# Performance work log

Hardware: AMD Instinct MI355X
Metric: run time of the kernel (lower is better)

The kernel has to match this reference:

```python
import jax, jax.numpy as jnp
import numpy as np

B, N, D = 128, 512, 256
NUM_TYPES, NUM_STATS = 6, 8
W_TYPE, W_STATS, W_CORR = 1.0, 1.0, 0.5
LN_EPS = 1e-5


def _mlp_head(x, W1, b1, g, be, W2, b2):
    # Linear -> GELU(exact) -> LayerNorm -> Linear (dropout is identity in eval)
    h = x @ W1 + b1
    h = jax.nn.gelu(h, approximate=False)
    mu = jnp.mean(h, axis=-1, keepdims=True)
    var = jnp.var(h, axis=-1, keepdims=True)
    h = (h - mu) / jnp.sqrt(var + LN_EPS) * g + be
    return h @ W2 + b2


def _masked_mean(x, m):
    m = m.astype(x.dtype)
    return jnp.sum(x * m) / jnp.maximum(jnp.sum(m), 1.0)


def setup_inputs() -> dict:
    key = jax.random.key(0)
    ks = jax.random.split(key, 16)
    s = 1.0 / np.sqrt(D)
    return {
        'column_embeddings': jax.random.normal(ks[0], (B, N, D), jnp.float32),
        'masked_columns': jax.random.uniform(ks[1], (B, N)) < 0.15,
        'type_targets': jax.random.randint(ks[2], (B, N), 0, NUM_TYPES),
        'column_statistics': jax.random.normal(ks[3], (B, N, NUM_STATS), jnp.float32),
        'column_correlations': jax.random.normal(ks[4], (B, N, N), jnp.float32),
        # type head params
        'Wt1': jax.random.normal(ks[5], (D, D), jnp.float32) * s,
        'bt1': jnp.zeros((D,), jnp.float32),
        'gt': jnp.ones((D,), jnp.float32),
        'blt': jnp.zeros((D,), jnp.float32),
        'Wt2': jax.random.normal(ks[6], (D, NUM_TYPES), jnp.float32) * s,
        'bt2': jnp.zeros((NUM_TYPES,), jnp.float32),
        # stats head params
        'Ws1': jax.random.normal(ks[7], (D, D), jnp.float32) * s,
        'bs1': jnp.zeros((D,), jnp.float32),
        'gs': jnp.ones((D,), jnp.float32),
        'bls': jnp.zeros((D,), jnp.float32),
        'Ws2': jax.random.normal(ks[8], (D, NUM_STATS), jnp.float32) * s,
        'bs2': jnp.zeros((NUM_STATS,), jnp.float32),
        # bilinear correlation head (nn.Bilinear(d,d,1) weight [1,d,d] -> [d,d])
        'Wc': jax.random.normal(ks[9], (D, D), jnp.float32) * s,
        'bc': jnp.zeros((), jnp.float32),
    }


def reference(column_embeddings, masked_columns, type_targets, column_statistics,
              column_correlations, Wt1, bt1, gt, blt, Wt2, bt2,
              Ws1, bs1, gs, bls, Ws2, bs2, Wc, bc):
    x = column_embeddings
    m = masked_columns

    type_logits = _mlp_head(x, Wt1, bt1, gt, blt, Wt2, bt2)   # [B,N,6]
    stats_preds = _mlp_head(x, Ws1, bs1, gs, bls, Ws2, bs2)   # [B,N,8]

    # fused bilinear correlation: replaces the O(N^2) python loop
    scores = jnp.einsum('bid,de,bje->bij', x, Wc, x) + bc     # [B,N,N]
    corr = jnp.tanh(scores)
    eye = jnp.eye(N, dtype=bool)
    corr = jnp.where(eye, jnp.ones((), corr.dtype), corr)

    # type loss: masked-mean cross-entropy
    logp = jax.nn.log_softmax(type_logits, axis=-1)
    nll = -jnp.take_along_axis(logp, type_targets[..., None], axis=-1)[..., 0]
    type_loss = _masked_mean(nll, m)

    # stats loss: masked-mean MSE over all stat elements of masked columns
    se = (stats_preds - column_statistics) ** 2
    stats_loss = _masked_mean(se, jnp.broadcast_to(m[:, :, None], se.shape))

    # correlation loss: mask is union over row/col masked columns
    m2 = m[:, :, None] | m[:, None, :]
    corr_loss = _masked_mean((corr - column_correlations) ** 2, m2)

    total = W_TYPE * type_loss + W_STATS * stats_loss + W_CORR * corr_loss
    return total
```

## Files before the change

### kernel.cpp

```cpp
#include <hip/hip_runtime.h>
#include <hip/hip_bf16.h>

#define BB 128
#define NN 512
#define DD 256

typedef __attribute__((ext_vector_type(4))) float f32x4;
typedef __attribute__((ext_vector_type(8))) short s16x8;
typedef __attribute__((ext_vector_type(8))) __bf16 bf16x8;

static __device__ __forceinline__ bf16x8 as_bf(s16x8 v) {
  return __builtin_bit_cast(bf16x8, v);
}

static __device__ __forceinline__ unsigned short f2bf(float f) {
  unsigned u = __builtin_bit_cast(unsigned, f);
  u += 0x7FFFu + ((u >> 16) & 1u);
  return (unsigned short)(u >> 16);
}

__device__ __forceinline__ float wave_sum(float v) {
#pragma unroll
  for (int o = 32; o > 0; o >>= 1) v += __shfl_xor(v, o);
  return v;
}

__global__ void k_init(int* wsi) {
  if (threadIdx.x < 8) wsi[threadIdx.x] = 0;
}

__global__ void k_counts(const int* __restrict__ msk, int* __restrict__ wsi) {
  const int b = blockIdx.x;
  int cnt = 0;
  for (int i = threadIdx.x; i < NN; i += blockDim.x) cnt += (msk[b * NN + i] != 0) ? 1 : 0;
  float s = wave_sum((float)cnt);
  __shared__ float red[4];
  const int lane = threadIdx.x & 63, wv = threadIdx.x >> 6;
  if (lane == 0) red[wv] = s;
  __syncthreads();
  if (threadIdx.x == 0) {
    int k = (int)(red[0] + red[1] + red[2] + red[3] + 0.5f);
    atomicAdd(&wsi[4], k);
    atomicAdd(&wsi[5], NN * NN - (NN - k) * (NN - k));
  }
}

__global__ void k_prep(const float* __restrict__ Wc, const float* __restrict__ Wt1,
                       const float* __restrict__ Ws1, const float* __restrict__ Wt2,
                       const float* __restrict__ Ws2,
                       unsigned short* __restrict__ WcT, unsigned short* __restrict__ Wt1T,
                       unsigned short* __restrict__ Ws1T, unsigned short* __restrict__ Wt2T,
                       unsigned short* __restrict__ Ws2T) {
  int t = blockIdx.x * 256 + threadIdx.x;
  int c = t >> 8, d = t & 255;
  WcT [c * 256 + d] = f2bf(Wc [d * 256 + c]);
  Wt1T[c * 256 + d] = f2bf(Wt1[d * 256 + c]);
  Ws1T[c * 256 + d] = f2bf(Ws1[d * 256 + c]);
  if (c < 16) {
    Wt2T[c * 256 + d] = (c < 6) ? f2bf(Wt2[d * 6 + c]) : (unsigned short)0;
    Ws2T[c * 256 + d] = (c < 8) ? f2bf(Ws2[d * 8 + c]) : (unsigned short)0;
  }
}

__global__ __launch_bounds__(512) void k_heads(
    const float* __restrict__ x, const int* __restrict__ msk,
    const int* __restrict__ tgt, const float* __restrict__ stats,
    const unsigned short* __restrict__ Wt1T, const unsigned short* __restrict__ Ws1T,
    const unsigned short* __restrict__ Wt2T, const unsigned short* __restrict__ Ws2T,
    const float* __restrict__ bt1, const float* __restrict__ bs1,
    const float* __restrict__ gt, const float* __restrict__ gs,
    const float* __restrict__ blt, const float* __restrict__ bls,
    const float* __restrict__ bt2, const float* __restrict__ bs2,
    float* __restrict__ fs)
{
  const int tid = threadIdx.x;
  const int lane = tid & 63, w = tid >> 6;
  const int wm = w & 1, wn = w >> 1;
  const int fr = lane & 15, fg = lane >> 4;
  const int row0 = blockIdx.x * 128;

  __shared__ __align__(16) unsigned short lds_h[128 * 264];
  __shared__ __align__(16) unsigned short lds_a[128 * 72];
  __shared__ __align__(16) unsigned short lds_b[256 * 72];
  __shared__ float sb1[2][256], sg[2][256], sbe[2][256];
  __shared__ float red[128 * 8];
  __shared__ float lg[128 * 16];

  if (tid < 256) { sb1[0][tid] = bt1[tid]; sg[0][tid] = gt[tid]; sbe[0][tid] = blt[tid]; }
  else { int t = tid - 256; sb1[1][t] = bs1[t]; sg[1][t] = gs[t]; sbe[1][t] = bls[t]; }

  f32x4 at[4][4], asx[4][4];
#pragma unroll
  for (int i = 0; i < 4; ++i)
#pragma unroll
    for (int j = 0; j < 4; ++j) {
      at[i][j]  = f32x4{0.f, 0.f, 0.f, 0.f};
      asx[i][j] = f32x4{0.f, 0.f, 0.f, 0.f};
    }

  for (int kt = 0; kt < 4; ++kt) {
    __syncthreads();
#pragma unroll
    for (int p = 0; p < 4; ++p) {
      int idx = tid + p * 512;
      int r = idx >> 4, c4 = idx & 15;
      float4 v = *(const float4*)&x[(size_t)(row0 + r) * DD + kt * 64 + c4 * 4];
      uint2 pk;
      pk.x = (unsigned)f2bf(v.x) | ((unsigned)f2bf(v.y) << 16);
      pk.y = (unsigned)f2bf(v.z) | ((unsigned)f2bf(v.w) << 16);
      *(uint2*)&lds_a[r * 72 + c4 * 4] = pk;
    }
#pragma unroll
    for (int p = 0; p < 4; ++p) {
      int idx = tid + p * 512;
      int r = idx >> 3, ch = idx & 7;
      *(uint4*)&lds_b[r * 72 + ch * 8] = *(const uint4*)&Wt1T[r * 256 + kt * 64 + ch * 8];
    }
    __syncthreads();
#pragma unroll
    for (int ks = 0; ks < 2; ++ks) {
      s16x8 af[4], bfv[4];
#pragma unroll
      for (int i = 0; i < 4; ++i)
        af[i] = *(const s16x8*)&lds_a[(wm * 64 + i * 16 + fr) * 72 + ks * 32 + fg * 8];
#pragma unroll
      for (int j = 0; j < 4; ++j)
        bfv[j] = *(const s16x8*)&lds_b[(wn * 64 + j * 16 + fr) * 72 + ks * 32 + fg * 8];
#pragma unroll
      for (int i = 0; i < 4; ++i)
#pragma unroll
        for (int j = 0; j < 4; ++j)
          at[i][j] = __builtin_amdgcn_mfma_f32_16x16x32_bf16(as_bf(af[i]), as_bf(bfv[j]), at[i][j], 0, 0, 0);
    }
    __syncthreads();
#pragma unroll
    for (int p = 0; p < 4; ++p) {
      int idx = tid + p * 512;
      int r = idx >> 3, ch = idx & 7;
      *(uint4*)&lds_b[r * 72 + ch * 8] = *(const uint4*)&Ws1T[r * 256 + kt * 64 + ch * 8];
    }
    __syncthreads();
#pragma unroll
    for (int ks = 0; ks < 2; ++ks) {
      s16x8 af[4], bfv[4];
#pragma unroll
      for (int i = 0; i < 4; ++i)
        af[i] = *(const s16x8*)&lds_a[(wm * 64 + i * 16 + fr) * 72 + ks * 32 + fg * 8];
#pragma unroll
      for (int j = 0; j < 4; ++j)
        bfv[j] = *(const s16x8*)&lds_b[(wn * 64 + j * 16 + fr) * 72 + ks * 32 + fg * 8];
#pragma unroll
      for (int i = 0; i < 4; ++i)
#pragma unroll
        for (int j = 0; j < 4; ++j)
          asx[i][j] = __builtin_amdgcn_mfma_f32_16x16x32_bf16(as_bf(af[i]), as_bf(bfv[j]), asx[i][j], 0, 0, 0);
    }
  }

  {
    float sA[16], qA[16];
#pragma unroll
    for (int k = 0; k < 16; ++k) { sA[k] = 0.f; qA[k] = 0.f; }
#pragma unroll
    for (int i = 0; i < 4; ++i)
#pragma unroll
      for (int j = 0; j < 4; ++j) {
        int col = wn * 64 + j * 16 + fr;
        float bb = sb1[0][col];
#pragma unroll
        for (int r = 0; r < 4; ++r) {
          float h = at[i][j][r] + bb;
          h = 0.5f * h * (1.0f + erff(h * 0.70710678118654752f));
          at[i][j][r] = h;
          sA[i * 4 + r] += h;
          qA[i * 4 + r] += h * h;
        }
      }
#pragma unroll
    for (int o = 1; o < 16; o <<= 1) {
#pragma unroll
      for (int k = 0; k < 16; ++k) {
        sA[k] += __shfl_xor(sA[k], o);
        qA[k] += __shfl_xor(qA[k], o);
      }
    }
    __syncthreads();
    if (fr == 0) {
#pragma unroll
      for (int i = 0; i < 4; ++i)
#pragma unroll
        for (int r = 0; r < 4; ++r) {
          int row = wm * 64 + i * 16 + fg * 4 + r;
          red[row * 8 + wn]     = sA[i * 4 + r];
          red[row * 8 + 4 + wn] = qA[i * 4 + r];
        }
    }
    __syncthreads();
#pragma unroll
    for (int i = 0; i < 4; ++i)
#pragma unroll
      for (int r = 0; r < 4; ++r) {
        int row = wm * 64 + i * 16 + fg * 4 + r;
        float s = red[row * 8 + 0] + red[row * 8 + 1] + red[row * 8 + 2] + red[row * 8 + 3];
        float q = red[row * 8 + 4] + red[row * 8 + 5] + red[row * 8 + 6] + red[row * 8 + 7];
        float mu = s * (1.0f / DD);
        float var = q * (1.0f / DD) - mu * mu;
        float rstd = rsqrtf(var + 1e-5f);
#pragma unroll
        for (int j = 0; j < 4; ++j) {
          int col = wn * 64 + j * 16 + fr;
          float hn = (at[i][j][r] - mu) * rstd * sg[0][col] + sbe[0][col];
          lds_h[row * 264 + col] = f2bf(hn);
        }
      }
    __syncthreads();
#pragma unroll
    for (int p = 0; p < 2; ++p) {
      int idx = tid + p * 512;
      int r = idx >> 6, c4 = idx & 63;
      *(uint2*)&lds_b[r * 264 + c4 * 4] = *(const uint2*)&Wt2T[r * 256 + c4 * 4];
    }
    __syncthreads();
    {
      f32x4 a1 = f32x4{0.f, 0.f, 0.f, 0.f};
#pragma unroll
      for (int ks = 0; ks < 8; ++ks) {
        s16x8 av = *(const s16x8*)&lds_h[(w * 16 + fr) * 264 + ks * 32 + fg * 8];
        s16x8 bv = *(const s16x8*)&lds_b[fr * 264 + ks * 32 + fg * 8];
        a1 = __builtin_amdgcn_mfma_f32_16x16x32_bf16(as_bf(av), as_bf(bv), a1, 0, 0, 0);
      }
#pragma unroll
      for (int r = 0; r < 4; ++r) lg[(w * 16 + fg * 4 + r) * 16 + fr] = a1[r];
    }
    __syncthreads();
    if (tid < 128) {
      int grow = row0 + tid;
      int mbit = msk[grow];
      float contrib = 0.0f;
      float l[6], mx = -1e30f;
#pragma unroll
      for (int c = 0; c < 6; ++c) { l[c] = lg[tid * 16 + c] + bt2[c]; mx = fmaxf(mx, l[c]); }
      float se = 0.0f;
#pragma unroll
      for (int c = 0; c < 6; ++c) se += expf(l[c] - mx);
      float lse = mx + logf(se);
      int t = tgt[grow];
      float lt = 0.0f;
#pragma unroll
      for (int c = 0; c < 6; ++c) lt = (c == t) ? l[c] : lt;
      contrib = mbit ? (lse - lt) : 0.0f;
      float s = wave_sum(contrib);
      if ((tid & 63) == 0) atomicAdd(&fs[0], s);
    }
    __syncthreads();
  }

  {
    float sA[16], qA[16];
#pragma unroll
    for (int k = 0; k < 16; ++k) { sA[k] = 0.f; qA[k] = 0.f; }
#pragma unroll
    for (int i = 0; i < 4; ++i)
#pragma unroll
      for (int j = 0; j < 4; ++j) {
        int col = wn * 64 + j * 16 + fr;
        float bb = sb1[1][col];
#pragma unroll
        for (int r = 0; r < 4; ++r) {
          float h = asx[i][j][r] + bb;
          h = 0.5f * h * (1.0f + erff(h * 0.70710678118654752f));
          asx[i][j][r] = h;
          sA[i * 4 + r] += h;
          qA[i * 4 + r] += h * h;
        }
      }
#pragma unroll
    for (int o = 1; o < 16; o <<= 1) {
#pragma unroll
      for (int k = 0; k < 16; ++k) {
        sA[k] += __shfl_xor(sA[k], o);
        qA[k] += __shfl_xor(qA[k], o);
      }
    }
    __syncthreads();
    if (fr == 0) {
#pragma unroll
      for (int i = 0; i < 4; ++i)
#pragma unroll
        for (int r = 0; r < 4; ++r) {
          int row = wm * 64 + i * 16 + fg * 4 + r;
          red[row * 8 + wn]     = sA[i * 4 + r];
          red[row * 8 + 4 + wn] = qA[i * 4 + r];
        }
    }
    __syncthreads();
#pragma unroll
    for (int i = 0; i < 4; ++i)
#pragma unroll
      for (int r = 0; r < 4; ++r) {
        int row = wm * 64 + i * 16 + fg * 4 + r;
        float s = red[row * 8 + 0] + red[row * 8 + 1] + red[row * 8 + 2] + red[row * 8 + 3];
        float q = red[row * 8 + 4] + red[row * 8 + 5] + red[row * 8 + 6] + red[row * 8 + 7];
        float mu = s * (1.0f / DD);
        float var = q * (1.0f / DD) - mu * mu;
        float rstd = rsqrtf(var + 1e-5f);
#pragma unroll
        for (int j = 0; j < 4; ++j) {
          int col = wn * 64 + j * 16 + fr;
          float hn = (asx[i][j][r] - mu) * rstd * sg[1][col] + sbe[1][col];
          lds_h[row * 264 + col] = f2bf(hn);
        }
      }
    __syncthreads();
#pragma unroll
    for (int p = 0; p < 2; ++p) {
      int idx = tid + p * 512;
      int r = idx >> 6, c4 = idx & 63;
      *(uint2*)&lds_b[r * 264 + c4 * 4] = *(const uint2*)&Ws2T[r * 256 + c4 * 4];
    }
    __syncthreads();
    {
      f32x4 a1 = f32x4{0.f, 0.f, 0.f, 0.f};
#pragma unroll
      for (int ks = 0; ks < 8; ++ks) {
        s16x8 av = *(const s16x8*)&lds_h[(w * 16 + fr) * 264 + ks * 32 + fg * 8];
        s16x8 bv = *(const s16x8*)&lds_b[fr * 264 + ks * 32 + fg * 8];
        a1 = __builtin_amdgcn_mfma_f32_16x16x32_bf16(as_bf(av), as_bf(bv), a1, 0, 0, 0);
      }
#pragma unroll
      for (int r = 0; r < 4; ++r) lg[(w * 16 + fg * 4 + r) * 16 + fr] = a1[r];
    }
    __syncthreads();
    if (tid < 128) {
      int grow = row0 + tid;
      int mbit = msk[grow];
      const float* st = stats + (size_t)grow * 8;
      float sse = 0.0f;
#pragma unroll
      for (int c = 0; c < 8; ++c) {
        float d = (lg[tid * 16 + c] + bs2[c]) - st[c];
        sse += d * d;
      }
      float contrib = mbit ? sse : 0.0f;
      float s = wave_sum(contrib);
      if ((tid & 63) == 0) atomicAdd(&fs[1], s);
    }
  }
}

__global__ __launch_bounds__(512) void k_corr(
    const float* __restrict__ x, const int* __restrict__ msk,
    const float* __restrict__ corr, const unsigned short* __restrict__ WcT,
    const float* __restrict__ bcp, float* __restrict__ fs)
{
  const int tid = threadIdx.x;
  const int b  = blockIdx.x >> 2;
  const int it = blockIdx.x & 3;
  const int i0 = it * 128;
  const int lane = tid & 63, w = tid >> 6;
  const int wm = w & 1, wn = w >> 1;
  const int fr = lane & 15, fg = lane >> 4;

  __shared__ __align__(16) unsigned short lds_y[128 * 264];
  __shared__ __align__(16) unsigned short lds_a[128 * 72];
  __shared__ __align__(16) unsigned short lds_b[256 * 72];
  __shared__ int ms_i[128];
  __shared__ int ms_j[256];
  __shared__ float red[8];

  const float* xb = x + (size_t)b * NN * DD;

  f32x4 acc[4][4];
#pragma unroll
  for (int i = 0; i < 4; ++i)
#pragma unroll
    for (int j = 0; j < 4; ++j) acc[i][j] = f32x4{0.f, 0.f, 0.f, 0.f};

  for (int kt = 0; kt < 4; ++kt) {
    __syncthreads();
#pragma unroll
    for (int p = 0; p < 4; ++p) {
      int idx = tid + p * 512;
      int r = idx >> 4, c4 = idx & 15;
      float4 v = *(const float4*)&xb[(size_t)(i0 + r) * DD + kt * 64 + c4 * 4];
      uint2 pk;
      pk.x = (unsigned)f2bf(v.x) | ((unsigned)f2bf(v.y) << 16);
      pk.y = (unsigned)f2bf(v.z) | ((unsigned)f2bf(v.w) << 16);
      *(uint2*)&lds_a[r * 72 + c4 * 4] = pk;
    }
#pragma unroll
    for (int p = 0; p < 4; ++p) {
      int idx = tid + p * 512;
      int r = idx >> 3, ch = idx & 7;
      *(uint4*)&lds_b[r * 72 + ch * 8] = *(const uint4*)&WcT[r * 256 + kt * 64 + ch * 8];
    }
    __syncthreads();
#pragma unroll
    for (int ks = 0; ks < 2; ++ks) {
      s16x8 af[4], bfv[4];
#pragma unroll
      for (int i = 0; i < 4; ++i)
        af[i] = *(const s16x8*)&lds_a[(wm * 64 + i * 16 + fr) * 72 + ks * 32 + fg * 8];
#pragma unroll
      for (int j = 0; j < 4; ++j)
        bfv[j] = *(const s16x8*)&lds_b[(wn * 64 + j * 16 + fr) * 72 + ks * 32 + fg * 8];
#pragma unroll
      for (int i = 0; i < 4; ++i)
#pragma unroll
        for (int j = 0; j < 4; ++j)
          acc[i][j] = __builtin_amdgcn_mfma_f32_16x16x32_bf16(as_bf(af[i]), as_bf(bfv[j]), acc[i][j], 0, 0, 0);
    }
  }
#pragma unroll
  for (int i = 0; i < 4; ++i)
#pragma unroll
    for (int j = 0; j < 4; ++j)
#pragma unroll
      for (int r = 0; r < 4; ++r) {
        int row = wm * 64 + i * 16 + fg * 4 + r;
        int col = wn * 64 + j * 16 + fr;
        lds_y[row * 264 + col] = f2bf(acc[i][j][r]);
      }
  if (tid < 128) ms_i[tid] = msk[b * NN + i0 + tid];

  const float bc = bcp[0];
  float sse = 0.0f;

  for (int jc = 0; jc < 2; ++jc) {
    const int j0 = jc * 256;
#pragma unroll
    for (int i = 0; i < 4; ++i)
#pragma unroll
      for (int j = 0; j < 4; ++j) acc[i][j] = f32x4{0.f, 0.f, 0.f, 0.f};

    for (int kt = 0; kt < 4; ++kt) {
      __syncthreads();
#pragma unroll
      for (int p = 0; p < 8; ++p) {
        int idx = tid + p * 512;
        int r = idx >> 4, c4 = idx & 15;
        float4 v = *(const float4*)&xb[(size_t)(j0 + r) * DD + kt * 64 + c4 * 4];
        uint2 pk;
        pk.x = (unsigned)f2bf(v.x) | ((unsigned)f2bf(v.y) << 16);
        pk.y = (unsigned)f2bf(v.z) | ((unsigned)f2bf(v.w) << 16);
        *(uint2*)&lds_b[r * 72 + c4 * 4] = pk;
      }
      if (kt == 0 && tid < 256) ms_j[tid] = msk[b * NN + j0 + tid];
      __syncthreads();
#pragma unroll
      for (int ks = 0; ks < 2; ++ks) {
        s16x8 af[4], bfv[4];
#pragma unroll
        for (int i = 0; i < 4; ++i)
          af[i] = *(const s16x8*)&lds_y[(wm * 64 + i * 16 + fr) * 264 + kt * 64 + ks * 32 + fg * 8];
#pragma unroll
        for (int j = 0; j < 4; ++j)
          bfv[j] = *(const s16x8*)&lds_b[(wn * 64 + j * 16 + fr) * 72 + ks * 32 + fg * 8];
#pragma unroll
        for (int i = 0; i < 4; ++i)
#pragma unroll
          for (int j = 0; j < 4; ++j)
            acc[i][j] = __builtin_amdgcn_mfma_f32_16x16x32_bf16(as_bf(af[i]), as_bf(bfv[j]), acc[i][j], 0, 0, 0);
      }
    }
    const float* tb = corr + (size_t)b * NN * NN;
#pragma unroll
    for (int i = 0; i < 4; ++i) {
      int rbase = wm * 64 + i * 16 + fg * 4;
#pragma unroll
      for (int j = 0; j < 4; ++j) {
        int colc = wn * 64 + j * 16 + fr;
        int gj = j0 + colc;
        int mj = ms_j[colc];
#pragma unroll
        for (int r = 0; r < 4; ++r) {
          int gi = i0 + rbase + r;
          float s = acc[i][j][r] + bc;
          float e = __expf(2.0f * s);
          float cv = 1.0f - 2.0f * __builtin_amdgcn_rcpf(e + 1.0f);
          if (gi == gj) cv = 1.0f;
          float tg = tb[(size_t)gi * NN + gj];
          float d = cv - tg;
          int mb = ms_i[rbase + r] | mj;
          sse += mb ? d * d : 0.0f;
        }
      }
    }
  }

  float s = wave_sum(sse);
  if (lane == 0) red[w] = s;
  __syncthreads();
  if (tid == 0) {
    float t = 0.f;
#pragma unroll
    for (int i = 0; i < 8; ++i) t += red[i];
    atomicAdd(&fs[2], t);
  }
}

__global__ void k_final(const float* __restrict__ fs, const int* __restrict__ wsi,
                        float* __restrict__ out) {
  if (threadIdx.x == 0 && blockIdx.x == 0) {
    float cm = (float)wsi[4];
    float c2 = (float)wsi[5];
    out[0] = fs[0] / fmaxf(cm, 1.0f) + fs[1] / fmaxf(8.0f * cm, 1.0f) +
             0.5f * fs[2] / fmaxf(c2, 1.0f);
  }
}

extern "C" void kernel_launch(void* const* d_in, const int* in_sizes, int n_in,
                              void* d_out, int out_size, void* d_ws, size_t ws_size,
                              hipStream_t stream) {
  const float* x     = (const float*)d_in[0];
  const int*   msk   = (const int*)d_in[1];
  const int*   tgt   = (const int*)d_in[2];
  const float* stats = (const float*)d_in[3];
  const float* corr  = (const float*)d_in[4];
  const float* Wt1   = (const float*)d_in[5];
  const float* bt1   = (const float*)d_in[6];
  const float* gt    = (const float*)d_in[7];
  const float* blt   = (const float*)d_in[8];
  const float* Wt2   = (const float*)d_in[9];
  const float* bt2   = (const float*)d_in[10];
  const float* Ws1   = (const float*)d_in[11];
  const float* bs1   = (const float*)d_in[12];
  const float* gs    = (const float*)d_in[13];
  const float* bls   = (const float*)d_in[14];
  const float* Ws2   = (const float*)d_in[15];
  const float* bs2   = (const float*)d_in[16];
  const float* Wc    = (const float*)d_in[17];
  const float* bc    = (const float*)d_in[18];

  float* fs = (float*)d_ws;
  int* wsi  = (int*)d_ws;
  unsigned short* WcT  = (unsigned short*)((char*)d_ws + 256);
  unsigned short* Wt1T = WcT + 65536;
  unsigned short* Ws1T = Wt1T + 65536;
  unsigned short* Wt2T = Ws1T + 65536;
  unsigned short* Ws2T = Wt2T + 4096;

  hipLaunchKernelGGL(k_init, dim3(1), dim3(64), 0, stream, wsi);
  hipLaunchKernelGGL(k_counts, dim3(BB), dim3(256), 0, stream, msk, wsi);
  hipLaunchKernelGGL(k_prep, dim3(256), dim3(256), 0, stream,
                     Wc, Wt1, Ws1, Wt2, Ws2, WcT, Wt1T, Ws1T, Wt2T, Ws2T);
  hipLaunchKernelGGL(k_heads, dim3((BB * NN) / 128), dim3(512), 0, stream,
                     x, msk, tgt, stats, Wt1T, Ws1T, Wt2T, Ws2T,
                     bt1, bs1, gt, gs, blt, bls, bt2, bs2, fs);
  hipLaunchKernelGGL(k_corr, dim3(BB * (NN / 128)), dim3(512), 0, stream,
                     x, msk, corr, WcT, bc, fs);
  hipLaunchKernelGGL(k_final, dim3(1), dim3(64), 0, stream, fs, wsi, (float*)d_out);
}
```

Baseline: 200.8 us.

## Pre-convert x to bf16 once and load MFMA operands directly from global

Adds a kernel that converts the fp32 embeddings to bf16 once in workspace, so the heads and correlation kernels no longer re-read and re-convert fp32 x. Both GEMM stages now load MFMA fragments straight from global or L2 instead of staging K-tiles through LDS, which removes many barriers and reduces LDS use, allowing higher occupancy. The two head GEMMs are computed sequentially with one shared accumulator set, lowering register pressure. The trade-off is an extra bf16 round trip of x through memory and uncoalesced 16-byte-per-lane global loads that depend on cache hits.

After: 342.2 us. 1.7x slower.

```diff
diff --git a/kernel.cpp b/kernel.cpp
--- a/kernel.cpp
+++ b/kernel.cpp
@@ -62,8 +62,20 @@
   }
 }
 
+__global__ void k_prep_x(const float* __restrict__ x, unsigned short* __restrict__ xbf) {
+  size_t i = ((size_t)blockIdx.x * 256 + threadIdx.x) * 8;
+  const float4* s = (const float4*)&x[i];
+  float4 v0 = s[0], v1 = s[1];
+  uint4 pk;
+  pk.x = (unsigned)f2bf(v0.x) | ((unsigned)f2bf(v0.y) << 16);
+  pk.y = (unsigned)f2bf(v0.z) | ((unsigned)f2bf(v0.w) << 16);
+  pk.z = (unsigned)f2bf(v1.x) | ((unsigned)f2bf(v1.y) << 16);
+  pk.w = (unsigned)f2bf(v1.z) | ((unsigned)f2bf(v1.w) << 16);
+  *(uint4*)&xbf[i] = pk;
+}
+
 __global__ __launch_bounds__(512) void k_heads(
-    const float* __restrict__ x, const int* __restrict__ msk,
+    const unsigned short* __restrict__ xbf, const int* __restrict__ msk,
     const int* __restrict__ tgt, const float* __restrict__ stats,
     const unsigned short* __restrict__ Wt1T, const unsigned short* __restrict__ Ws1T,
     const unsigned short* __restrict__ Wt2T, const unsigned short* __restrict__ Ws2T,
@@ -79,85 +91,38 @@
   const int fr = lane & 15, fg = lane >> 4;
   const int row0 = blockIdx.x * 128;
 
-  __shared__ __align__(16) unsigned short lds_h[128 * 264];
-  __shared__ __align__(16) unsigned short lds_a[128 * 72];
-  __shared__ __align__(16) unsigned short lds_b[256 * 72];
-  __shared__ float sb1[2][256], sg[2][256], sbe[2][256];
-  __shared__ float red[128 * 8];
-  __shared__ float lg[128 * 16];
-
-  if (tid < 256) { sb1[0][tid] = bt1[tid]; sg[0][tid] = gt[tid]; sbe[0][tid] = blt[tid]; }
-  else { int t = tid - 256; sb1[1][t] = bs1[t]; sg[1][t] = gs[t]; sbe[1][t] = bls[t]; }
-
-  f32x4 at[4][4], asx[4][4];
-#pragma unroll
-  for (int i = 0; i < 4; ++i)
-#pragma unroll
-    for (int j = 0; j < 4; ++j) {
-      at[i][j]  = f32x4{0.f, 0.f, 0.f, 0.f};
-      asx[i][j] = f32x4{0.f, 0.f, 0.f, 0.f};
-    }
-
-  for (int kt = 0; kt < 4; ++kt) {
-    __syncthreads();
-#pragma unroll
-    for (int p = 0; p < 4; ++p) {
-      int idx = tid + p * 512;
-      int r = idx >> 4, c4 = idx & 15;
-      float4 v = *(const float4*)&x[(size_t)(row0 + r) * DD + kt * 64 + c4 * 4];
-      uint2 pk;
-      pk.x = (unsigned)f2bf(v.x) | ((unsigned)f2bf(v.y) << 16);
-      pk.y = (unsigned)f2bf(v.z) | ((unsigned)f2bf(v.w) << 16);
-      *(uint2*)&lds_a[r * 72 + c4 * 4] = pk;
-    }
-#pragma unroll
-    for (int p = 0; p < 4; ++p) {
-      int idx = tid + p * 512;
-      int r = idx >> 3, ch = idx & 7;
-      *(uint4*)&lds_b[r * 72 + ch * 8] = *(const uint4*)&Wt1T[r * 256 + kt * 64 + ch * 8];
-    }
-    __syncthreads();
-#pragma unroll
-    for (int ks = 0; ks < 2; ++ks) {
+  __shared__ __align__(16) unsigned short pool[33792 + 4224];
+  __shared__ float lg[128 * 8];
+  unsigned short* lds_h  = pool;
+  unsigned short* lds_w2 = pool + 33792;
+  float* red = (float*)(pool + 33792);
+
+  const unsigned short* xrow = xbf + (size_t)row0 * DD;
+
+  {
+    f32x4 acc[4][4];
+#pragma unroll
+    for (int i = 0; i < 4; ++i)
+#pragma unroll
+      for (int j = 0; j < 4; ++j) acc[i][j] = f32x4{0.f, 0.f, 0.f, 0.f};
+
+#pragma unroll
+    for (int ks = 0; ks < 8; ++ks) {
+      const int ko = ks * 32 + fg * 8;
       s16x8 af[4], bfv[4];
 #pragma unroll
       for (int i = 0; i < 4; ++i)
-        af[i] = *(const s16x8*)&lds_a[(wm * 64 + i * 16 + fr) * 72 + ks * 32 + fg * 8];
+        af[i] = *(const s16x8*)&xrow[(size_t)(wm * 64 + i * 16 + fr) * DD + ko];
 #pragma unroll
       for (int j = 0; j < 4; ++j)
-        bfv[j] = *(const s16x8*)&lds_b[(wn * 64 + j * 16 + fr) * 72 + ks * 32 + fg * 8];
+        bfv[j] = *(const s16x8*)&Wt1T[(size_t)(wn * 64 + j * 16 + fr) * DD + ko];
 #pragma unroll
       for (int i = 0; i < 4; ++i)
 #pragma unroll
         for (int j = 0; j < 4; ++j)
-          at[i][j] = __builtin_amdgcn_mfma_f32_16x16x32_bf16(as_bf(af[i]), as_bf(bfv[j]), at[i][j], 0, 0, 0);
-    }
-    __syncthreads();
-#pragma unroll
-    for (int p = 0; p < 4; ++p) {
-      int idx = tid + p * 512;
-      int r = idx >> 3, ch = idx & 7;
-      *(uint4*)&lds_b[r * 72 + ch * 8] = *(const uint4*)&Ws1T[r * 256 + kt * 64 + ch * 8];
-    }
-    __syncthreads();
-#pragma unroll
-    for (int ks = 0; ks < 2; ++ks) {
-      s16x8 af[4], bfv[4];
-#pragma unroll
-      for (int i = 0; i < 4; ++i)
-        af[i] = *(const s16x8*)&lds_a[(wm * 64 + i * 16 + fr) * 72 + ks * 32 + fg * 8];
-#pragma unroll
-      for (int j = 0; j < 4; ++j)
-        bfv[j] = *(const s16x8*)&lds_b[(wn * 64 + j * 16 + fr) * 72 + ks * 32 + fg * 8];
-#pragma unroll
-      for (int i = 0; i < 4; ++i)
-#pragma unroll
-        for (int j = 0; j < 4; ++j)
-          asx[i][j] = __builtin_amdgcn_mfma_f32_16x16x32_bf16(as_bf(af[i]), as_bf(bfv[j]), asx[i][j], 0, 0, 0);
-    }
-  }
-
-  {
+          acc[i][j] = __builtin_amdgcn_mfma_f32_16x16x32_bf16(as_bf(af[i]), as_bf(bfv[j]), acc[i][j], 0, 0, 0);
+    }
+
     float sA[16], qA[16];
 #pragma unroll
     for (int k = 0; k < 16; ++k) { sA[k] = 0.f; qA[k] = 0.f; }
@@ -166,12 +131,12 @@
 #pragma unroll
       for (int j = 0; j < 4; ++j) {
         int col = wn * 64 + j * 16 + fr;
-        float bb = sb1[0][col];
+        float bb = bt1[col];
 #pragma unroll
         for (int r = 0; r < 4; ++r) {
-          float h = at[i][j][r] + bb;
+          float h = acc[i][j][r] + bb;
           h = 0.5f * h * (1.0f + erff(h * 0.70710678118654752f));
-          at[i][j][r] = h;
+          acc[i][j][r] = h;
           sA[i * 4 + r] += h;
           qA[i * 4 + r] += h * h;
         }
@@ -184,7 +149,6 @@
         qA[k] += __shfl_xor(qA[k], o);
       }
     }
-    __syncthreads();
     if (fr == 0) {
 #pragma unroll
       for (int i = 0; i < 4; ++i)
@@ -209,16 +173,14 @@
 #pragma unroll
         for (int j = 0; j < 4; ++j) {
           int col = wn * 64 + j * 16 + fr;
-          float hn = (at[i][j][r] - mu) * rstd * sg[0][col] + sbe[0][col];
+          float hn = (acc[i][j][r] - mu) * rstd * gt[col] + blt[col];
           lds_h[row * 264 + col] = f2bf(hn);
         }
       }
     __syncthreads();
-#pragma unroll
-    for (int p = 0; p < 2; ++p) {
-      int idx = tid + p * 512;
-      int r = idx >> 6, c4 = idx & 63;
-      *(uint2*)&lds_b[r * 264 + c4 * 4] = *(const uint2*)&Wt2T[r * 256 + c4 * 4];
+    {
+      int r = tid >> 5, ch = tid & 31;
+      *(uint4*)&lds_w2[r * 264 + ch * 8] = *(const uint4*)&Wt2T[r * 256 + ch * 8];
     }
     __syncthreads();
     {
@@ -226,20 +188,21 @@
 #pragma unroll
       for (int ks = 0; ks < 8; ++ks) {
         s16x8 av = *(const s16x8*)&lds_h[(w * 16 + fr) * 264 + ks * 32 + fg * 8];
-        s16x8 bv = *(const s16x8*)&lds_b[fr * 264 + ks * 32 + fg * 8];
+        s16x8 bv = *(const s16x8*)&lds_w2[fr * 264 + ks * 32 + fg * 8];
         a1 = __builtin_amdgcn_mfma_f32_16x16x32_bf16(as_bf(av), as_bf(bv), a1, 0, 0, 0);
       }
-#pragma unroll
-      for (int r = 0; r < 4; ++r) lg[(w * 16 + fg * 4 + r) * 16 + fr] = a1[r];
+      if (fr < 8) {
+#pragma unroll
+        for (int r = 0; r < 4; ++r) lg[(w * 16 + fg * 4 + r) * 8 + fr] = a1[r];
+      }
     }
     __syncthreads();
     if (tid < 128) {
       int grow = row0 + tid;
       int mbit = msk[grow];
-      float contrib = 0.0f;
       float l[6], mx = -1e30f;
 #pragma unroll
-      for (int c = 0; c < 6; ++c) { l[c] = lg[tid * 16 + c] + bt2[c]; mx = fmaxf(mx, l[c]); }
+      for (int c = 0; c < 6; ++c) { l[c] = lg[tid * 8 + c] + bt2[c]; mx = fmaxf(mx, l[c]); }
       float se = 0.0f;
 #pragma unroll
       for (int c = 0; c < 6; ++c) se += expf(l[c] - mx);
@@ -248,7 +211,7 @@
       float lt = 0.0f;
 #pragma unroll
       for (int c = 0; c < 6; ++c) lt = (c == t) ? l[c] : lt;
-      contrib = mbit ? (lse - lt) : 0.0f;
+      float contrib = mbit ? (lse - lt) : 0.0f;
       float s = wave_sum(contrib);
       if ((tid & 63) == 0) atomicAdd(&fs[0], s);
     }
@@ -256,6 +219,29 @@
   }
 
   {
+    f32x4 acc[4][4];
+#pragma unroll
+    for (int i = 0; i < 4; ++i)
+#pragma unroll
+      for (int j = 0; j < 4; ++j) acc[i][j] = f32x4{0.f, 0.f, 0.f, 0.f};
+
+#pragma unroll
+    for (int ks = 0; ks < 8; ++ks) {
+      const int ko = ks * 32 + fg * 8;
+      s16x8 af[4], bfv[4];
+#pragma unroll
+      for (int i = 0; i < 4; ++i)
+        af[i] = *(const s16x8*)&xrow[(size_t)(wm * 64 + i * 16 + fr) * DD + ko];
+#pragma unroll
+      for (int j = 0; j < 4; ++j)
+        bfv[j] = *(const s16x8*)&Ws1T[(size_t)(wn * 64 + j * 16 + fr) * DD + ko];
+#pragma unroll
+      for (int i = 0; i < 4; ++i)
+#pragma unroll
+        for (int j = 0; j < 4; ++j)
+          acc[i][j] = __builtin_amdgcn_mfma_f32_16x16x32_bf16(as_bf(af[i]), as_bf(bfv[j]), acc[i][j], 0, 0, 0);
+    }
+
     float sA[16], qA[16];
 #pragma unroll
     for (int k = 0; k < 16; ++k) { sA[k] = 0.f; qA[k] = 0.f; }
@@ -264,12 +250,12 @@
 #pragma unroll
       for (int j = 0; j < 4; ++j) {
         int col = wn * 64 + j * 16 + fr;
-        float bb = sb1[1][col];
+        float bb = bs1[col];
 #pragma unroll
         for (int r = 0; r < 4; ++r) {
-          float h = asx[i][j][r] + bb;
+          float h = acc[i][j][r] + bb;
           h = 0.5f * h * (1.0f + erff(h * 0.70710678118654752f));
-          asx[i][j][r] = h;
+          acc[i][j][r] = h;
           sA[i * 4 + r] += h;
           qA[i * 4 + r] += h * h;
         }
@@ -282,7 +268,6 @@
         qA[k] += __shfl_xor(qA[k], o);
       }
     }
-    __syncthreads();
     if (fr == 0) {
 #pragma unroll
       for (int i = 0; i < 4; ++i)
@@ -307,16 +292,14 @@
 #pragma unroll
         for (int j = 0; j < 4; ++j) {
           int col = wn * 64 + j * 16 + fr;
-          float hn = (asx[i][j][r] - mu) * rstd * sg[1][col] + sbe[1][col];
+          float hn = (acc[i][j][r] - mu) * rstd * gs[col] + bls[col];
           lds_h[row * 264 + col] = f2bf(hn);
         }
       }
     __syncthreads();
-#pragma unroll
-    for (int p = 0; p < 2; ++p) {
-      int idx = tid + p * 512;
-      int r = idx >> 6, c4 = idx & 63;
-      *(uint2*)&lds_b[r * 264 + c4 * 4] = *(const uint2*)&Ws2T[r * 256 + c4 * 4];
+    {
+      int r = tid >> 5, ch = tid & 31;
+      *(uint4*)&lds_w2[r * 264 + ch * 8] = *(const uint4*)&Ws2T[r * 256 + ch * 8];
     }
     __syncthreads();
     {
@@ -324,11 +307,13 @@
 #pragma unroll
       for (int ks = 0; ks < 8; ++ks) {
         s16x8 av = *(const s16x8*)&lds_h[(w * 16 + fr) * 264 + ks * 32 + fg * 8];
-        s16x8 bv = *(const s16x8*)&lds_b[fr * 264 + ks * 32 + fg * 8];
+        s16x8 bv = *(const s16x8*)&lds_w2[fr * 264 + ks * 32 + fg * 8];
         a1 = __builtin_amdgcn_mfma_f32_16x16x32_bf16(as_bf(av), as_bf(bv), a1, 0, 0, 0);
       }
-#pragma unroll
-      for (int r = 0; r < 4; ++r) lg[(w * 16 + fg * 4 + r) * 16 + fr] = a1[r];
+      if (fr < 8) {
+#pragma unroll
+        for (int r = 0; r < 4; ++r) lg[(w * 16 + fg * 4 + r) * 8 + fr] = a1[r];
+      }
     }
     __syncthreads();
     if (tid < 128) {
@@ -338,7 +323,7 @@
       float sse = 0.0f;
 #pragma unroll
       for (int c = 0; c < 8; ++c) {
-        float d = (lg[tid * 16 + c] + bs2[c]) - st[c];
+        float d = (lg[tid * 8 + c] + bs2[c]) - st[c];
         sse += d * d;
       }
       float contrib = mbit ? sse : 0.0f;
@@ -349,7 +334,7 @@
 }
 
 __global__ __launch_bounds__(512) void k_corr(
-    const float* __restrict__ x, const int* __restrict__ msk,
+    const unsigned short* __restrict__ xbf, const int* __restrict__ msk,
     const float* __restrict__ corr, const unsigned short* __restrict__ WcT,
     const float* __restrict__ bcp, float* __restrict__ fs)
 {
@@ -362,13 +347,11 @@
   const int fr = lane & 15, fg = lane >> 4;
 
   __shared__ __align__(16) unsigned short lds_y[128 * 264];
-  __shared__ __align__(16) unsigned short lds_a[128 * 72];
-  __shared__ __align__(16) unsigned short lds_b[256 * 72];
   __shared__ int ms_i[128];
-  __shared__ int ms_j[256];
-  __shared__ float red[8];
-
-  const float* xb = x + (size_t)b * NN * DD;
+  __shared__ int ms_j[512];
+  __shared__ float red8[8];
+
+  const unsigned short* xb = xbf + (size_t)b * NN * DD;
 
   f32x4 acc[4][4];
 #pragma unroll
@@ -376,40 +359,21 @@
 #pragma unroll
     for (int j = 0; j < 4; ++j) acc[i][j] = f32x4{0.f, 0.f, 0.f, 0.f};
 
-  for (int kt = 0; kt < 4; ++kt) {
-    __syncthreads();
-#pragma unroll
-    for (int p = 0; p < 4; ++p) {
-      int idx = tid + p * 512;
-      int r = idx >> 4, c4 = idx & 15;
-      float4 v = *(const float4*)&xb[(size_t)(i0 + r) * DD + kt * 64 + c4 * 4];
-      uint2 pk;
-      pk.x = (unsigned)f2bf(v.x) | ((unsigned)f2bf(v.y) << 16);
-      pk.y = (unsigned)f2bf(v.z) | ((unsigned)f2bf(v.w) << 16);
-      *(uint2*)&lds_a[r * 72 + c4 * 4] = pk;
-    }
-#pragma unroll
-    for (int p = 0; p < 4; ++p) {
-      int idx = tid + p * 512;
-      int r = idx >> 3, ch = idx & 7;
-      *(uint4*)&lds_b[r * 72 + ch * 8] = *(const uint4*)&WcT[r * 256 + kt * 64 + ch * 8];
-    }
-    __syncthreads();
-#pragma unroll
-    for (int ks = 0; ks < 2; ++ks) {
-      s16x8 af[4], bfv[4];
-#pragma unroll
-      for (int i = 0; i < 4; ++i)
-        af[i] = *(const s16x8*)&lds_a[(wm * 64 + i * 16 + fr) * 72 + ks * 32 + fg * 8];
+#pragma unroll
+  for (int ks = 0; ks < 8; ++ks) {
+    const int ko = ks * 32 + fg * 8;
+    s16x8 af[4], bfv[4];
+#pragma unroll
+    for (int i = 0; i < 4; ++i)
+      af[i] = *(const s16x8*)&xb[(size_t)(i0 + wm * 64 + i * 16 + fr) * DD + ko];
+#pragma unroll
+    for (int j = 0; j < 4; ++j)
+      bfv[j] = *(const s16x8*)&WcT[(size_t)(wn * 64 + j * 16 + fr) * DD + ko];
+#pragma unroll
+    for (int i = 0; i < 4; ++i)
 #pragma unroll
       for (int j = 0; j < 4; ++j)
-        bfv[j] = *(const s16x8*)&lds_b[(wn * 64 + j * 16 + fr) * 72 + ks * 32 + fg * 8];
-#pragma unroll
-      for (int i = 0; i < 4; ++i)
-#pragma unroll
-        for (int j = 0; j < 4; ++j)
-          acc[i][j] = __builtin_amdgcn_mfma_f32_16x16x32_bf16(as_bf(af[i]), as_bf(bfv[j]), acc[i][j], 0, 0, 0);
-    }
+        acc[i][j] = __builtin_amdgcn_mfma_f32_16x16x32_bf16(as_bf(af[i]), as_bf(bfv[j]), acc[i][j], 0, 0, 0);
   }
 #pragma unroll
   for (int i = 0; i < 4; ++i)
@@ -422,8 +386,11 @@
         lds_y[row * 264 + col] = f2bf(acc[i][j][r]);
       }
   if (tid < 128) ms_i[tid] = msk[b * NN + i0 + tid];
+  ms_j[tid] = msk[b * NN + tid];
+  __syncthreads();
 
   const float bc = bcp[0];
+  const float* tb = corr + (size_t)b * NN * NN;
   float sse = 0.0f;
 
   for (int jc = 0; jc < 2; ++jc) {
@@ -433,37 +400,22 @@
 #pragma unroll
       for (int j = 0; j < 4; ++j) acc[i][j] = f32x4{0.f, 0.f, 0.f, 0.f};
 
-    for (int kt = 0; kt < 4; ++kt) {
-      __syncthreads();
-#pragma unroll
-      for (int p = 0; p < 8; ++p) {
-        int idx = tid + p * 512;
-        int r = idx >> 4, c4 = idx & 15;
-        float4 v = *(const float4*)&xb[(size_t)(j0 + r) * DD + kt * 64 + c4 * 4];
-        uint2 pk;
-        pk.x = (unsigned)f2bf(v.x) | ((unsigned)f2bf(v.y) << 16);
-        pk.y = (unsigned)f2bf(v.z) | ((unsigned)f2bf(v.w) << 16);
-        *(uint2*)&lds_b[r * 72 + c4 * 4] = pk;
-      }
-      if (kt == 0 && tid < 256) ms_j[tid] = msk[b * NN + j0 + tid];
-      __syncthreads();
-#pragma unroll
-      for (int ks = 0; ks < 2; ++ks) {
-        s16x8 af[4], bfv[4];
-#pragma unroll
-        for (int i = 0; i < 4; ++i)
-          af[i] = *(const s16x8*)&lds_y[(wm * 64 + i * 16 + fr) * 264 + kt * 64 + ks * 32 + fg * 8];
+#pragma unroll
+    for (int ks = 0; ks < 8; ++ks) {
+      const int ko = ks * 32 + fg * 8;
+      s16x8 af[4], bfv[4];
+#pragma unroll
+      for (int i = 0; i < 4; ++i)
+        af[i] = *(const s16x8*)&lds_y[(wm * 64 + i * 16 + fr) * 264 + ko];
+#pragma unroll
+      for (int j = 0; j < 4; ++j)
+        bfv[j] = *(const s16x8*)&xb[(size_t)(j0 + wn * 64 + j * 16 + fr) * DD + ko];
+#pragma unroll
+      for (int i = 0; i < 4; ++i)
 #pragma unroll
         for (int j = 0; j < 4; ++j)
-          bfv[j] = *(const s16x8*)&lds_b[(wn * 64 + j * 16 + fr) * 72 + ks * 32 + fg * 8];
-#pragma unroll
-        for (int i = 0; i < 4; ++i)
-#pragma unroll
-          for (int j = 0; j < 4; ++j)
-            acc[i][j] = __builtin_amdgcn_mfma_f32_16x16x32_bf16(as_bf(af[i]), as_bf(bfv[j]), acc[i][j], 0, 0, 0);
-      }
-    }
-    const float* tb = corr + (size_t)b * NN * NN;
+          acc[i][j] = __builtin_amdgcn_mfma_f32_16x16x32_bf16(as_bf(af[i]), as_bf(bfv[j]), acc[i][j], 0, 0, 0);
+    }
 #pragma unroll
     for (int i = 0; i < 4; ++i) {
       int rbase = wm * 64 + i * 16 + fg * 4;
@@ -471,7 +423,7 @@
       for (int j = 0; j < 4; ++j) {
         int colc = wn * 64 + j * 16 + fr;
         int gj = j0 + colc;
-        int mj = ms_j[colc];
+        int mj = ms_j[gj];
 #pragma unroll
         for (int r = 0; r < 4; ++r) {
           int gi = i0 + rbase + r;
@@ -489,12 +441,12 @@
   }
 
   float s = wave_sum(sse);
-  if (lane == 0) red[w] = s;
+  if (lane == 0) red8[w] = s;
   __syncthreads();
   if (tid == 0) {
     float t = 0.f;
 #pragma unroll
-    for (int i = 0; i < 8; ++i) t += red[i];
+    for (int i = 0; i < 8; ++i) t += red8[i];
     atomicAdd(&fs[2], t);
   }
 }
@@ -539,15 +491,17 @@
   unsigned short* Ws1T = Wt1T + 65536;
   unsigned short* Wt2T = Ws1T + 65536;
   unsigned short* Ws2T = Wt2T + 4096;
+  unsigned short* xbf  = Ws2T + 4096;
 
   hipLaunchKernelGGL(k_init, dim3(1), dim3(64), 0, stream, wsi);
   hipLaunchKernelGGL(k_counts, dim3(BB), dim3(256), 0, stream, msk, wsi);
   hipLaunchKernelGGL(k_prep, dim3(256), dim3(256), 0, stream,
                      Wc, Wt1, Ws1, Wt2, Ws2, WcT, Wt1T, Ws1T, Wt2T, Ws2T);
+  hipLaunchKernelGGL(k_prep_x, dim3((BB * NN * DD) / (256 * 8)), dim3(256), 0, stream, x, xbf);
   hipLaunchKernelGGL(k_heads, dim3((BB * NN) / 128), dim3(512), 0, stream,
-                     x, msk, tgt, stats, Wt1T, Ws1T, Wt2T, Ws2T,
+                     xbf, msk, tgt, stats, Wt1T, Ws1T, Wt2T, Ws2T,
                      bt1, bs1, gt, gs, blt, bls, bt2, bs2, fs);
   hipLaunchKernelGGL(k_corr, dim3(BB * (NN / 128)), dim3(512), 0, stream,
-                     x, msk, corr, WcT, bc, fs);
+                     xbf, msk, corr, WcT, bc, fs);
   hipLaunchKernelGGL(k_final, dim3(1), dim3(64), 0, stream, fs, wsi, (float*)d_out);
 }
```
